# Kernel tuning notes

Measured on AMD Instinct MI355X. Metric: run time of the kernel, lower is better.

Reference implementation:

```python
import jax, jax.numpy as jnp
import numpy as np


def setup_inputs() -> dict:
    key = jax.random.key(0)
    k1, k2, k3 = jax.random.split(key, 3)
    B, C, E, L, W = 4, 2, 256, 16000, 40
    mixture_w = jax.random.normal(k1, (B, E, L), dtype=jnp.float32)
    est_mask = jax.random.uniform(k2, (B, C, E, L), dtype=jnp.float32)
    basis_w = jax.random.normal(k3, (W, E), dtype=jnp.float32) * (1.0 / np.sqrt(E))
    return {"mixture_w": mixture_w, "est_mask": est_mask, "basis_w": basis_w}


def overlap_and_add(frames, frame_step):
    # frames: [B, C, L, W] -> [B, C, T] with T = (L-1)*frame_step + W
    B, C, L, W = frames.shape
    T = (L - 1) * frame_step + W
    # scatter-add each frame into the output waveform at its strided offset
    idx = (jnp.arange(L)[:, None] * frame_step + jnp.arange(W)[None, :]).reshape(-1)
    out = jnp.zeros((B, C, T), dtype=frames.dtype)
    return out.at[..., idx].add(frames.reshape(B, C, L * W))


def reference(mixture_w, est_mask, basis_w):
    # mixture_w: [B, E, L], est_mask: [B, C, E, L], basis_w: [W, E]
    source_w = mixture_w[:, None, :, :] * est_mask          # [B, C, E, L]
    # transpose(2,3) then Linear(E->W): contract over E
    est_frames = jnp.einsum('bcel,we->bclw', source_w, basis_w)  # [B, C, L, W]
    W = basis_w.shape[0]
    return overlap_and_add(est_frames, W // 2)              # [B, C, T]
```

## Files before the change

### kernel.cpp

```cpp
#include <hip/hip_runtime.h>

#define BQ   4
#define CQ   2
#define EQ   256
#define LQ   16000
#define WQ   40
#define STEP 20
#define TQ   ((LQ - 1) * STEP + WQ)
#define TLF  63
#define OWN  (TLF * STEP)
#define NBX  254
#define NH   4
#define EH   (EQ / NH)
#define SPAN (TLF * STEP + WQ + STEP)

__global__ void transpose_basis_kernel(const float* __restrict__ basis,
                                       float* __restrict__ wsT) {
    int i = blockIdx.x * 256 + threadIdx.x;
    if (i < EQ * WQ) {
        int e = i / WQ;
        int w = i - e * WQ;
        wsT[i] = basis[w * EQ + e];
    }
}

__global__ __launch_bounds__(512, 8) void decoder_kernel(
    const float* __restrict__ mix,
    const float* __restrict__ mask,
    const float* __restrict__ wsT,
    float* __restrict__ out)
{
    __shared__ float outS[2][CQ][SPAN];

    const int tid = threadIdx.x;
    const int ll  = tid & 63;
    const int c   = (tid >> 6) & 1;
    const int h   = __builtin_amdgcn_readfirstlane(tid >> 7);
    const int bx  = blockIdx.x;
    const int b   = blockIdx.y;
    const int f   = TLF * bx - 1 + ll;

    const int   fc    = min(max(f, 0), LQ - 1);
    const float valid = (f >= 0 && f < LQ) ? 1.0f : 0.0f;

    float acc[WQ];
#pragma unroll
    for (int w = 0; w < WQ; ++w) acc[w] = 0.0f;

    const float* mp = mix  + ((size_t)b * EQ + h * EH) * LQ + fc;
    const float* kp = mask + (((size_t)(b * CQ + c)) * EQ + h * EH) * LQ + fc;
    const float* bp = wsT + (size_t)h * EH * WQ;

    for (int eo = 0; eo < EH; eo += 2) {
        float m0 = mp[(size_t)eo * LQ];
        float m1 = mp[(size_t)(eo + 1) * LQ];
        float k0 = kp[(size_t)eo * LQ] * valid;
        float k1 = kp[(size_t)(eo + 1) * LQ] * valid;
        {
            float s = m0 * k0;
            const float* bb = bp + eo * WQ;
#pragma unroll
            for (int w = 0; w < WQ; ++w) acc[w] = fmaf(s, bb[w], acc[w]);
        }
        {
            float s = m1 * k1;
            const float* bb = bp + (eo + 1) * WQ;
#pragma unroll
            for (int w = 0; w < WQ; ++w) acc[w] = fmaf(s, bb[w], acc[w]);
        }
    }

    const int base = ll * STEP;
    const int cp   = h >> 1;
    const int hp   = h & 1;
    if (hp == 0 && (ll & 1) == 0) {
#pragma unroll
        for (int w = 0; w < WQ; ++w) outS[cp][c][base + w] = acc[w];
    }
    __syncthreads();
    if (hp == 0 && (ll & 1) == 1) {
#pragma unroll
        for (int w = 0; w < WQ; ++w) outS[cp][c][base + w] += acc[w];
    }
    __syncthreads();
    if (hp == 1 && (ll & 1) == 0) {
#pragma unroll
        for (int w = 0; w < WQ; ++w) outS[cp][c][base + w] += acc[w];
    }
    __syncthreads();
    if (hp == 1 && (ll & 1) == 1) {
#pragma unroll
        for (int w = 0; w < WQ; ++w) outS[cp][c][base + w] += acc[w];
    }
    __syncthreads();

    for (int cc = 0; cc < CQ; ++cc) {
        const size_t ob = ((size_t)b * CQ + cc) * TQ + (size_t)OWN * bx;
        for (int i = tid; i < OWN; i += 512) {
            const long t = (long)OWN * bx + i;
            if (t < (long)TQ) {
                out[ob + i] = outS[0][cc][STEP + i] + outS[1][cc][STEP + i];
            }
        }
    }
}

extern "C" void kernel_launch(void* const* d_in, const int* in_sizes, int n_in,
                              void* d_out, int out_size, void* d_ws, size_t ws_size,
                              hipStream_t stream) {
    const float* mix   = (const float*)d_in[0];
    const float* mask  = (const float*)d_in[1];
    const float* basis = (const float*)d_in[2];
    float* out = (float*)d_out;
    float* wsT = (float*)d_ws;

    transpose_basis_kernel<<<dim3((EQ * WQ + 255) / 256), 256, 0, stream>>>(basis, wsT);

    dim3 grid(NBX, BQ);
    decoder_kernel<<<grid, 512, 0, stream>>>(mix, mask, wsT, out);
}
```

Before: 242.7 us.

## Give each thread the full E reduction and move channel split to grid

Work is redistributed across threads and blocks. Each thread now reduces over all 256 channels, so the E dimension is no longer split into four parts that must be combined through shared memory. Each block covers 255 frames for a single (batch, source) pair, with the source taken from grid z. This removes the cross-split shared-memory reduction and the extra barriers, and reloads of mixture data are now per source rather than shared. The cost is a longer serial loop per thread and a much smaller grid (504 blocks of 256 threads), which may leave the GPU underoccupied.

```diff
diff --git a/kernel.cpp b/kernel.cpp
--- a/kernel.cpp
+++ b/kernel.cpp
@@ -7,12 +7,10 @@
 #define WQ   40
 #define STEP 20
 #define TQ   ((LQ - 1) * STEP + WQ)
-#define TLF  63
+#define TLF  255
 #define OWN  (TLF * STEP)
-#define NBX  254
-#define NH   4
-#define EH   (EQ / NH)
-#define SPAN (TLF * STEP + WQ + STEP)
+#define NBX  63
+#define SPAN (TLF * STEP + WQ)
 
 __global__ void transpose_basis_kernel(const float* __restrict__ basis,
                                        float* __restrict__ wsT) {
@@ -24,20 +22,19 @@
     }
 }
 
-__global__ __launch_bounds__(512, 8) void decoder_kernel(
+__global__ __launch_bounds__(256, 4) void decoder_kernel(
     const float* __restrict__ mix,
     const float* __restrict__ mask,
     const float* __restrict__ wsT,
     float* __restrict__ out)
 {
-    __shared__ float outS[2][CQ][SPAN];
+    __shared__ float outS[SPAN];
 
     const int tid = threadIdx.x;
-    const int ll  = tid & 63;
-    const int c   = (tid >> 6) & 1;
-    const int h   = __builtin_amdgcn_readfirstlane(tid >> 7);
+    const int ll  = tid;
     const int bx  = blockIdx.x;
     const int b   = blockIdx.y;
+    const int c   = blockIdx.z;
     const int f   = TLF * bx - 1 + ll;
 
     const int   fc    = min(max(f, 0), LQ - 1);
@@ -47,60 +44,42 @@
 #pragma unroll
     for (int w = 0; w < WQ; ++w) acc[w] = 0.0f;
 
-    const float* mp = mix  + ((size_t)b * EQ + h * EH) * LQ + fc;
-    const float* kp = mask + (((size_t)(b * CQ + c)) * EQ + h * EH) * LQ + fc;
-    const float* bp = wsT + (size_t)h * EH * WQ;
+    const float* mp = mix  + (size_t)b * EQ * LQ + fc;
+    const float* kp = mask + ((size_t)(b * CQ + c)) * EQ * LQ + fc;
 
-    for (int eo = 0; eo < EH; eo += 2) {
-        float m0 = mp[(size_t)eo * LQ];
-        float m1 = mp[(size_t)(eo + 1) * LQ];
-        float k0 = kp[(size_t)eo * LQ] * valid;
-        float k1 = kp[(size_t)(eo + 1) * LQ] * valid;
-        {
-            float s = m0 * k0;
-            const float* bb = bp + eo * WQ;
+    for (int eo = 0; eo < EQ; eo += 4) {
+        float m[4], k[4];
 #pragma unroll
-            for (int w = 0; w < WQ; ++w) acc[w] = fmaf(s, bb[w], acc[w]);
+        for (int u = 0; u < 4; ++u) {
+            m[u] = mp[(size_t)(eo + u) * LQ];
+            k[u] = kp[(size_t)(eo + u) * LQ];
         }
-        {
-            float s = m1 * k1;
-            const float* bb = bp + (eo + 1) * WQ;
+#pragma unroll
+        for (int u = 0; u < 4; ++u) {
+            const float s  = m[u] * k[u] * valid;
+            const float* bb = wsT + (eo + u) * WQ;
 #pragma unroll
             for (int w = 0; w < WQ; ++w) acc[w] = fmaf(s, bb[w], acc[w]);
         }
     }
 
     const int base = ll * STEP;
-    const int cp   = h >> 1;
-    const int hp   = h & 1;
-    if (hp == 0 && (ll & 1) == 0) {
+    if ((ll & 1) == 0) {
 #pragma unroll
-        for (int w = 0; w < WQ; ++w) outS[cp][c][base + w] = acc[w];
+        for (int w = 0; w < WQ; ++w) outS[base + w] = acc[w];
     }
     __syncthreads();
-    if (hp == 0 && (ll & 1) == 1) {
+    if (ll & 1) {
 #pragma unroll
-        for (int w = 0; w < WQ; ++w) outS[cp][c][base + w] += acc[w];
-    }
-    __syncthreads();
-    if (hp == 1 && (ll & 1) == 0) {
-#pragma unroll
-        for (int w = 0; w < WQ; ++w) outS[cp][c][base + w] += acc[w];
-    }
-    __syncthreads();
-    if (hp == 1 && (ll & 1) == 1) {
-#pragma unroll
-        for (int w = 0; w < WQ; ++w) outS[cp][c][base + w] += acc[w];
+        for (int w = 0; w < WQ; ++w) outS[base + w] += acc[w];
     }
     __syncthreads();
 
-    for (int cc = 0; cc < CQ; ++cc) {
-        const size_t ob = ((size_t)b * CQ + cc) * TQ + (size_t)OWN * bx;
-        for (int i = tid; i < OWN; i += 512) {
-            const long t = (long)OWN * bx + i;
-            if (t < (long)TQ) {
-                out[ob + i] = outS[0][cc][STEP + i] + outS[1][cc][STEP + i];
-            }
+    const size_t ob = ((size_t)b * CQ + c) * TQ + (size_t)OWN * bx;
+    for (int i = tid; i < OWN; i += 256) {
+        const long t = (long)OWN * bx + i;
+        if (t < (long)TQ) {
+            out[ob + i] = outS[STEP + i];
         }
     }
 }
@@ -116,6 +95,6 @@
 
     transpose_basis_kernel<<<dim3((EQ * WQ + 255) / 256), 256, 0, stream>>>(basis, wsT);
 
-    dim3 grid(NBX, BQ);
-    decoder_kernel<<<grid, 512, 0, stream>>>(mix, mask, wsT, out);
+    dim3 grid(NBX, BQ, CQ);
+    decoder_kernel<<<grid, 256, 0, stream>>>(mix, mask, wsT, out);
 }
```

Measured after the change: 283.4 us. 1.17x slower.
